# Kernel tuning notes

Measured on AMD Instinct MI355X. Metric: run time of the kernel, lower is better.

The kernel has to match this reference:

```python
import jax, jax.numpy as jnp
import numpy as np
from jax import lax

SEQ_LEN, INPUT_DIM, NUM_HIDDEN, NUM_CLASSES, BATCH = 512, 1, 1024, 10, 512


def setup_inputs() -> dict:
    key = jax.random.key(0)
    k_x, k_hx, k_hh, k_ph = jax.random.split(key, 4)
    xav = lambda k, shape: jax.random.normal(k, shape, dtype=jnp.float32) * np.sqrt(2.0 / (shape[0] + shape[1]))
    return {
        "x": jax.random.normal(k_x, (BATCH, SEQ_LEN), dtype=jnp.float32),
        "W_hx": xav(k_hx, (NUM_HIDDEN, INPUT_DIM)),
        "W_hh": xav(k_hh, (NUM_HIDDEN, NUM_HIDDEN)),
        "W_ph": xav(k_ph, (NUM_CLASSES, NUM_HIDDEN)),
        "b_h": jnp.zeros((BATCH,), dtype=jnp.float32),
        "b_p": jnp.zeros((BATCH,), dtype=jnp.float32),
    }


def reference(x, W_hx, W_hh, W_ph, b_h, b_p):
    # x: [B, T]; hidden state h: [H, B] (matches torch code layout)
    H = W_hh.shape[0]
    B = x.shape[0]
    h0 = jnp.zeros((H, B), dtype=x.dtype)
    xs = x.T  # [T, B]: scan over time

    def step(h, x_t):
        # W_hx @ x_t[None, :] : [H,1] @ [1,B] -> [H,B]; b_h broadcasts over last axis
        h_new = jnp.tanh(W_hx @ x_t[None, :] + W_hh @ h + b_h)
        return h_new, None

    h_final, _ = lax.scan(step, h0, xs)
    p_t = W_ph @ h_final + b_p  # [C, B]
    return p_t.T  # [B, C]
```

## Files before the change

kernel.cpp:

```cpp
#include <hip/hip_runtime.h>
#include <hip/hip_fp16.h>

#define H 1024
#define B 512
#define T 512
#define NC 10

#define NGROUPS 16
#define WPG 16
#define NSLICE 32
#define MROWS 64
#define FLAG_STRIDE 16
#define NT 512

typedef _Float16 f16x8 __attribute__((ext_vector_type(8)));
typedef _Float16 f16x4 __attribute__((ext_vector_type(4)));
typedef float    f32x4 __attribute__((ext_vector_type(4)));
typedef unsigned u32x4 __attribute__((ext_vector_type(4)));
typedef unsigned long long ull;

__device__ __forceinline__ float fast_tanh(float x) {
    float e = __expf(2.0f * x);
    return 1.0f - 2.0f / (e + 1.0f);
}

__global__ void convert_w(const float* __restrict__ w, _Float16* __restrict__ o) {
    int i = (blockIdx.x * 256 + threadIdx.x) * 4;
    float4 v = *(const float4*)(w + i);
    f16x4 r;
    r[0] = (_Float16)v.x; r[1] = (_Float16)v.y;
    r[2] = (_Float16)v.z; r[3] = (_Float16)v.w;
    *(f16x4*)(o + i) = r;
}

__global__ void transpose_x(const float* __restrict__ x, float* __restrict__ xT) {
    __shared__ float tile[32][33];
    const int tx = threadIdx.x & 31;
    const int ty = threadIdx.x >> 5;
    const int t0 = blockIdx.x * 32;
    const int b0 = blockIdx.y * 32;
    #pragma unroll
    for (int i = ty; i < 32; i += 8)
        tile[i][tx] = x[(size_t)(b0 + i) * T + t0 + tx];
    __syncthreads();
    #pragma unroll
    for (int i = ty; i < 32; i += 8)
        xT[(size_t)(t0 + i) * B + b0 + tx] = tile[tx][i];
}

#define G_LOAD_X4(dst, addr, OFF) \
    asm volatile("global_load_dwordx4 %0, %1, off offset:" OFF " sc0" \
                 : "=&v"(dst) : "v"(addr) : "memory")

#define ISSUE8(arr, base) do { \
    G_LOAD_X4(arr[0], (base), "0");   G_LOAD_X4(arr[1], (base), "64");  \
    G_LOAD_X4(arr[2], (base), "128"); G_LOAD_X4(arr[3], (base), "192"); \
    G_LOAD_X4(arr[4], (base), "256"); G_LOAD_X4(arr[5], (base), "320"); \
    G_LOAD_X4(arr[6], (base), "384"); G_LOAD_X4(arr[7], (base), "448"); \
} while (0)

#define G_STORE_X2(addr, data) \
    asm volatile("global_store_dwordx2 %0, %1, off sc0" \
                 :: "v"(addr), "v"(data) : "memory")

#define PISSUE(v) \
    asm volatile("global_load_dword %0, %1, off sc0 sc1" \
                 : "=&v"(v) : "v"(fpoll) : "memory")

__global__ void __launch_bounds__(NT, 1) rnn_persist(
        const _Float16* __restrict__ Wf, const float* __restrict__ xT,
        const float* __restrict__ Whx, const float* __restrict__ bh,
        _Float16* h0, _Float16* h1, unsigned* flags, unsigned* claim) {

    __shared__ _Float16 Wlds[MROWS * H];
    __shared__ f32x4 red[6][4][64];
    __shared__ int s_g, s_ms;

    const int tid  = threadIdx.x;
    const int wave = tid >> 6;
    const int lane = tid & 63;
    const int lm   = lane & 15;
    const int kg   = lane >> 4;
    const int wk   = wave >> 1;
    const int wn   = wave & 1;

    if (tid == 0) {
        unsigned xcd;
        asm volatile("s_getreg_b32 %0, hwreg(HW_REG_XCC_ID)" : "=s"(xcd));
        xcd &= 7;
        unsigned slot = atomicAdd(&claim[xcd], 1u);
        s_ms = (int)(slot & 15);
        s_g  = (int)(xcd * 2 + (slot >> 4));
    }
    __syncthreads();
    const int g  = s_g;
    const int ms = s_ms;

    for (int f = tid; f < MROWS * H / 8; f += NT) {
        const int p   = f >> 6;
        const int l   = f & 63;
        const int kkb = p >> 2;
        const int pwm = (p >> 1) & 1;
        const int prb = p & 1;
        const int pkg = l >> 4;
        const int plm = l & 15;
        const int m = ms * 64 + pwm * 32 + prb * 16 + plm;
        f16x8 v = *(const f16x8*)(Wf + (size_t)m * H + kkb * 32 + pkg * 8);
        *(f16x8*)((char*)Wlds + (size_t)f * 16) = v;
    }
    __syncthreads();

    const int n = g * NSLICE + wn * 16 + lm;
    float whx[4][4];
    #pragma unroll
    for (int mf = 0; mf < 4; ++mf)
        #pragma unroll
        for (int r = 0; r < 4; ++r)
            whx[mf][r] = Whx[ms * 64 + (mf >> 1) * 32 + (mf & 1) * 16 + kg * 4 + r];
    const float bhn = bh[n];

    const ull hu0 = (ull)h0, hu1 = (ull)h1;
    const char* abase = (const char*)Wlds + (size_t)wk * 32768 + lane * 16;

    const ull fpoll = (ull)(flags +
        (size_t)((((g << 4) | ms) << 4) | (lane & 15)) * FLAG_STRIDE);
    unsigned* fpub = flags +
        (size_t)((((g << 4) | (lane & 15)) << 4) | ms) * FLAG_STRIDE;

    #define KSTEP(KB, CNT) do {                                               \
        asm volatile("s_waitcnt vmcnt(" CNT ")" ::: "memory");                \
        __builtin_amdgcn_sched_barrier(0);                                    \
        f16x8 a0 = *(const f16x8*)(abase + KB * 4096);                        \
        f16x8 a1 = *(const f16x8*)(abase + KB * 4096 + 1024);                 \
        f16x8 a2 = *(const f16x8*)(abase + KB * 4096 + 2048);                 \
        f16x8 a3 = *(const f16x8*)(abase + KB * 4096 + 3072);                 \
        union { u32x4 u; f16x8 v; } bb; bb.u = hB[KB];                        \
        acc0 = __builtin_amdgcn_mfma_f32_16x16x32_f16(a0, bb.v, acc0, 0,0,0); \
        acc1 = __builtin_amdgcn_mfma_f32_16x16x32_f16(a1, bb.v, acc1, 0,0,0); \
        acc2 = __builtin_amdgcn_mfma_f32_16x16x32_f16(a2, bb.v, acc2, 0,0,0); \
        acc3 = __builtin_amdgcn_mfma_f32_16x16x32_f16(a3, bb.v, acc3, 0,0,0); \
    } while (0)

    #define EPI(ACC, MF, OFF) do {                                            \
        union { ull u; f16x4 v; } s_;                                         \
        _Pragma("unroll")                                                     \
        for (int r = 0; r < 4; ++r)                                           \
            s_.v[r] = (_Float16)fast_tanh(ACC[r] + whx[MF][r] * xn + bhn);    \
        G_STORE_X2(wr + OFF, s_.u);                                           \
    } while (0)

    for (int t = 0; t < T; ++t) {
        if (wave == 0 && t) {
            const unsigned tc = (unsigned)t;
            unsigned va, vb;
            PISSUE(va); PISSUE(vb);
            for (;;) {
                asm volatile("s_waitcnt vmcnt(1)" ::: "memory");
                __builtin_amdgcn_sched_barrier(0);
                if (__all((int)(va >= tc))) break;
                PISSUE(va);
                asm volatile("s_waitcnt vmcnt(1)" ::: "memory");
                __builtin_amdgcn_sched_barrier(0);
                if (__all((int)(vb >= tc))) break;
                PISSUE(vb);
            }
            asm volatile("s_waitcnt vmcnt(0)" ::: "memory");
            __builtin_amdgcn_sched_barrier(0);
        }
        __syncthreads();
        __builtin_amdgcn_sched_barrier(0);

        const ull rdb = (t & 1) ? hu1 : hu0;
        const ull wrb = (t & 1) ? hu0 : hu1;
        const ull rd  = rdb + (size_t)n * 2048 + wk * 512 + kg * 16;

        u32x4 hB[8];
        f32x4 acc0 = {0.f, 0.f, 0.f, 0.f};
        f32x4 acc1 = {0.f, 0.f, 0.f, 0.f};
        f32x4 acc2 = {0.f, 0.f, 0.f, 0.f};
        f32x4 acc3 = {0.f, 0.f, 0.f, 0.f};

        ISSUE8(hB, rd);
        KSTEP(0, "7"); KSTEP(1, "6"); KSTEP(2, "5"); KSTEP(3, "4");
        KSTEP(4, "3"); KSTEP(5, "2"); KSTEP(6, "1"); KSTEP(7, "0");

        if (wk) {
            const int ri = (wk - 1) * 2 + wn;
            red[ri][0][lane] = acc0;
            red[ri][1][lane] = acc1;
            red[ri][2][lane] = acc2;
            red[ri][3][lane] = acc3;
        }
        __syncthreads();

        if (wk == 0) {
            const float xn = xT[(size_t)t * B + n];
            #pragma unroll
            for (int j = 0; j < 3; ++j) {
                const int ri = j * 2 + wn;
                acc0 += red[ri][0][lane];
                acc1 += red[ri][1][lane];
                acc2 += red[ri][2][lane];
                acc3 += red[ri][3][lane];
            }
            const ull wr = wrb + (size_t)n * 2048 + (size_t)(ms * 128) + kg * 8;
            EPI(acc0, 0, 0);
            EPI(acc1, 1, 32);
            EPI(acc2, 2, 64);
            EPI(acc3, 3, 96);
            asm volatile("s_waitcnt vmcnt(0)" ::: "memory");
        }
        __syncthreads();
        if (wave == 0 && lane < 16)
            __hip_atomic_store(fpub, (unsigned)(t + 1),
                               __ATOMIC_RELAXED, __HIP_MEMORY_SCOPE_AGENT);
        __builtin_amdgcn_sched_barrier(0);
    }
    #undef KSTEP
    #undef EPI
}

__global__ void proj_kernel(const _Float16* __restrict__ hT,
                            const float* __restrict__ Wph,
                            const float* __restrict__ bp,
                            float* __restrict__ out) {
    const int b = blockIdx.x;
    const int lane = threadIdx.x;
    float partial[NC];
    #pragma unroll
    for (int c = 0; c < NC; ++c) partial[c] = 0.f;
    for (int i = lane; i < H; i += 64) {
        float hv = (float)hT[(size_t)b * H + i];
        #pragma unroll
        for (int c = 0; c < NC; ++c) partial[c] += Wph[(size_t)c * H + i] * hv;
    }
    #pragma unroll
    for (int c = 0; c < NC; ++c) {
        float v = partial[c];
        #pragma unroll
        for (int off = 32; off; off >>= 1) v += __shfl_down(v, off);
        if (lane == 0) out[(size_t)b * NC + c] = v + bp[b];
    }
}

extern "C" void kernel_launch(void* const* d_in, const int* in_sizes, int n_in,
                              void* d_out, int out_size, void* d_ws, size_t ws_size,
                              hipStream_t stream) {
    const float* x   = (const float*)d_in[0];
    const float* Whx = (const float*)d_in[1];
    const float* Whh = (const float*)d_in[2];
    const float* Wph = (const float*)d_in[3];
    const float* bh  = (const float*)d_in[4];
    const float* bp  = (const float*)d_in[5];
    float* out = (float*)d_out;

    char* ws = (char*)d_ws;
    _Float16* Wf    = (_Float16*)ws;
    _Float16* h0    = (_Float16*)(ws + (2u << 20));
    _Float16* h1    = (_Float16*)(ws + (3u << 20));
    float*    xT    = (float*)(ws + (4u << 20));
    unsigned* flags = (unsigned*)(ws + (5u << 20));
    unsigned* claim = (unsigned*)(ws + (5u << 20) + 262144);

    convert_w<<<(H * H / 4) / 256, 256, 0, stream>>>(Whh, Wf);
    transpose_x<<<dim3(T / 32, B / 32), 256, 0, stream>>>(x, xT);
    hipMemsetAsync(h0, 0, (size_t)B * H * 2, stream);
    hipMemsetAsync(flags, 0, 262144 + 256, stream);

    rnn_persist<<<NGROUPS * WPG, NT, 0, stream>>>(Wf, xT, Whx, bh,
                                                  h0, h1, flags, claim);

    proj_kernel<<<B, 64, 0, stream>>>(h0, Wph, bp, out);
}
```

Before: 2.140 ms.

## Distribute split-K reduction and epilogue across all waves; poll flags per wave

Replaces the wave-0-only reduction of split-K MFMA partials with an all-to-all exchange, so each k-group wave reduces and applies tanh to one of the four M fragments and stores its own slice. Every wave now polls only the producer flags it needs, which removes the barrier at the top of each timestep. The aim is to shorten the serial epilogue and sync chain on the recurrent critical path. In exchange every wave issues global flag polls, and correctness relies on each wave's own polling covering the h data it reads.

```diff
diff --git a/kernel.cpp b/kernel.cpp
--- a/kernel.cpp
+++ b/kernel.cpp
@@ -73,7 +73,7 @@
         _Float16* h0, _Float16* h1, unsigned* flags, unsigned* claim) {
 
     __shared__ _Float16 Wlds[MROWS * H];
-    __shared__ f32x4 red[6][4][64];
+    __shared__ f32x4 red[12][2][64];
     __shared__ int s_g, s_ms;
 
     const int tid  = threadIdx.x;
@@ -111,19 +111,17 @@
     __syncthreads();
 
     const int n = g * NSLICE + wn * 16 + lm;
-    float whx[4][4];
-    #pragma unroll
-    for (int mf = 0; mf < 4; ++mf)
-        #pragma unroll
-        for (int r = 0; r < 4; ++r)
-            whx[mf][r] = Whx[ms * 64 + (mf >> 1) * 32 + (mf & 1) * 16 + kg * 4 + r];
+    float whxm[4];
+    #pragma unroll
+    for (int r = 0; r < 4; ++r)
+        whxm[r] = Whx[ms * 64 + (wk >> 1) * 32 + (wk & 1) * 16 + kg * 4 + r];
     const float bhn = bh[n];
 
     const ull hu0 = (ull)h0, hu1 = (ull)h1;
     const char* abase = (const char*)Wlds + (size_t)wk * 32768 + lane * 16;
 
     const ull fpoll = (ull)(flags +
-        (size_t)((((g << 4) | ms) << 4) | (lane & 15)) * FLAG_STRIDE);
+        (size_t)((((g << 4) | ms) << 4) | (wk * 4 + (lane & 3))) * FLAG_STRIDE);
     unsigned* fpub = flags +
         (size_t)((((g << 4) | (lane & 15)) << 4) | ms) * FLAG_STRIDE;
 
@@ -141,16 +139,8 @@
         acc3 = __builtin_amdgcn_mfma_f32_16x16x32_f16(a3, bb.v, acc3, 0,0,0); \
     } while (0)
 
-    #define EPI(ACC, MF, OFF) do {                                            \
-        union { ull u; f16x4 v; } s_;                                         \
-        _Pragma("unroll")                                                     \
-        for (int r = 0; r < 4; ++r)                                           \
-            s_.v[r] = (_Float16)fast_tanh(ACC[r] + whx[MF][r] * xn + bhn);    \
-        G_STORE_X2(wr + OFF, s_.u);                                           \
-    } while (0)
-
     for (int t = 0; t < T; ++t) {
-        if (wave == 0 && t) {
+        if (t) {
             const unsigned tc = (unsigned)t;
             unsigned va, vb;
             PISSUE(va); PISSUE(vb);
@@ -167,8 +157,6 @@
             asm volatile("s_waitcnt vmcnt(0)" ::: "memory");
             __builtin_amdgcn_sched_barrier(0);
         }
-        __syncthreads();
-        __builtin_amdgcn_sched_barrier(0);
 
         const ull rdb = (t & 1) ? hu1 : hu0;
         const ull wrb = (t & 1) ? hu0 : hu1;
@@ -184,32 +172,45 @@
         KSTEP(0, "7"); KSTEP(1, "6"); KSTEP(2, "5"); KSTEP(3, "4");
         KSTEP(4, "3"); KSTEP(5, "2"); KSTEP(6, "1"); KSTEP(7, "0");
 
-        if (wk) {
-            const int ri = (wk - 1) * 2 + wn;
-            red[ri][0][lane] = acc0;
-            red[ri][1][lane] = acc1;
-            red[ri][2][lane] = acc2;
-            red[ri][3][lane] = acc3;
+        f32x4 mine;
+        if (wk == 0) {
+            red[0][wn][lane] = acc1; red[1][wn][lane] = acc2;
+            red[2][wn][lane] = acc3; mine = acc0;
+        } else if (wk == 1) {
+            red[3][wn][lane] = acc0; red[4][wn][lane] = acc2;
+            red[5][wn][lane] = acc3; mine = acc1;
+        } else if (wk == 2) {
+            red[6][wn][lane] = acc0; red[7][wn][lane] = acc1;
+            red[8][wn][lane] = acc3; mine = acc2;
+        } else {
+            red[9][wn][lane] = acc0; red[10][wn][lane] = acc1;
+            red[11][wn][lane] = acc2; mine = acc3;
         }
         __syncthreads();
 
+        const float xn = xT[(size_t)t * B + n];
         if (wk == 0) {
-            const float xn = xT[(size_t)t * B + n];
-            #pragma unroll
-            for (int j = 0; j < 3; ++j) {
-                const int ri = j * 2 + wn;
-                acc0 += red[ri][0][lane];
-                acc1 += red[ri][1][lane];
-                acc2 += red[ri][2][lane];
-                acc3 += red[ri][3][lane];
-            }
-            const ull wr = wrb + (size_t)n * 2048 + (size_t)(ms * 128) + kg * 8;
-            EPI(acc0, 0, 0);
-            EPI(acc1, 1, 32);
-            EPI(acc2, 2, 64);
-            EPI(acc3, 3, 96);
-            asm volatile("s_waitcnt vmcnt(0)" ::: "memory");
+            mine += red[3][wn][lane]; mine += red[6][wn][lane];
+            mine += red[9][wn][lane];
+        } else if (wk == 1) {
+            mine += red[0][wn][lane]; mine += red[7][wn][lane];
+            mine += red[10][wn][lane];
+        } else if (wk == 2) {
+            mine += red[1][wn][lane]; mine += red[4][wn][lane];
+            mine += red[11][wn][lane];
+        } else {
+            mine += red[2][wn][lane]; mine += red[5][wn][lane];
+            mine += red[8][wn][lane];
         }
+        union { ull u; f16x4 v; } s_;
+        #pragma unroll
+        for (int r = 0; r < 4; ++r)
+            s_.v[r] = (_Float16)fast_tanh(mine[r] + whxm[r] * xn + bhn);
+        const ull wr = wrb + (size_t)n * 2048
+                     + (size_t)(ms * 128) + wk * 32 + kg * 8;
+        G_STORE_X2(wr, s_.u);
+        asm volatile("s_waitcnt vmcnt(0)" ::: "memory");
+
         __syncthreads();
         if (wave == 0 && lane < 16)
             __hip_atomic_store(fpub, (unsigned)(t + 1),
@@ -217,7 +218,6 @@
         __builtin_amdgcn_sched_barrier(0);
     }
     #undef KSTEP
-    #undef EPI
 }
 
 __global__ void proj_kernel(const _Float16* __restrict__ hT,
```

Result: faster. 2.065 ms (-3.5%).
